# Kernel optimization log

Hardware: AMD Instinct MI355X
Metric: run time of the kernel (lower is better)

Reference implementation:

```python
import jax, jax.numpy as jnp
import numpy as np

D_MODEL = 1024
NHEAD = 16
HEAD_DIM = D_MODEL // NHEAD


def setup_inputs() -> dict:
    key = jax.random.key(0)
    ks = jax.random.split(key, 11)
    B, T = 2, 2048
    s = 1.0 / np.sqrt(D_MODEL)
    return {
        "query": jax.random.normal(ks[0], (B, T, D_MODEL), jnp.float32),
        "key": jax.random.normal(ks[1], (B, T, D_MODEL), jnp.float32),
        "value": jax.random.normal(ks[2], (B, T, D_MODEL), jnp.float32),
        "Wq": jax.random.normal(ks[3], (D_MODEL, D_MODEL), jnp.float32) * s,
        "bq": jnp.zeros((D_MODEL,), jnp.float32),
        "Wk": jax.random.normal(ks[4], (D_MODEL, D_MODEL), jnp.float32) * s,
        "bk": jnp.zeros((D_MODEL,), jnp.float32),
        "Wv": jax.random.normal(ks[5], (D_MODEL, D_MODEL), jnp.float32) * s,
        "bv": jnp.zeros((D_MODEL,), jnp.float32),
        "Wo": jax.random.normal(ks[6], (D_MODEL, D_MODEL), jnp.float32) * s,
        "bo": jnp.zeros((D_MODEL,), jnp.float32),
    }


def reference(query, key, value, Wq, bq, Wk, bk, Wv, bv, Wo, bo):
    B, T, _ = query.shape
    scale = HEAD_DIM ** -0.5
    # Linear projections (torch Linear: x @ W.T + b)
    Q = query @ Wq.T + bq
    K = key @ Wk.T + bk
    V = value @ Wv.T + bv
    # [B, H, T, hd]
    Q = Q.reshape(B, T, NHEAD, HEAD_DIM).transpose(0, 2, 1, 3)
    K = K.reshape(B, T, NHEAD, HEAD_DIM).transpose(0, 2, 1, 3)
    V = V.reshape(B, T, NHEAD, HEAD_DIM).transpose(0, 2, 1, 3)
    # Attention scores [B, H, T, T]
    scores = jnp.einsum("bhqd,bhkd->bhqk", Q, K) * scale
    probs = jax.nn.softmax(scores, axis=-1)
    # dropout is identity in eval mode
    out = jnp.einsum("bhqk,bhkd->bhqd", probs, V)
    out = out.transpose(0, 2, 1, 3).reshape(B, T, D_MODEL)
    return out @ Wo.T + bo
```

## Files before the change

kernel.cpp:

```cpp
#include <hip/hip_runtime.h>
#include <stdint.h>

#define LOG2E_OVER_SQRTHD 0.18033688011112042f
#define SM_BIAS 12.0f

typedef unsigned short u16;
typedef _Float16 f16;
typedef __attribute__((ext_vector_type(4))) float f32x4;
typedef __attribute__((ext_vector_type(8))) _Float16 f16x8;

static __device__ __forceinline__ u16 f2h_bits(float f) {
  union { f16 h; u16 u; } v; v.h = (f16)f; return v.u;
}

static __device__ __forceinline__ void g2l16(const void* g, void* l) {
  __builtin_amdgcn_global_load_lds((const __attribute__((address_space(1))) void*)g,
                                   (__attribute__((address_space(3))) void*)l,
                                   16, 0, 0);
}

__global__ __launch_bounds__(256) void pack_x3(const float* __restrict__ q,
    const float* __restrict__ k, const float* __restrict__ v, u16* __restrict__ dst) {
  int z = blockIdx.y;
  const float* src = (z == 0) ? q : (z == 1) ? k : v;
  u16* d = dst + (size_t)z * 4096 * 1024;
  int idx = blockIdx.x * 256 + threadIdx.x;
  float4 x = ((const float4*)src)[idx];
  ushort4 o;
  o.x = f2h_bits(x.x); o.y = f2h_bits(x.y); o.z = f2h_bits(x.z); o.w = f2h_bits(x.w);
  *(ushort4*)(d + (size_t)idx * 4) = o;
}

__global__ __launch_bounds__(256) void pack_w4(const float* __restrict__ wq,
    const float* __restrict__ wk, const float* __restrict__ wv,
    const float* __restrict__ wo, u16* __restrict__ dst) {
  int z = blockIdx.y;
  const float* src = (z == 0) ? wq : (z == 1) ? wk : (z == 2) ? wv : wo;
  u16* d = dst + (size_t)z * 1024 * 1024;
  int idx = blockIdx.x * 256 + threadIdx.x;
  float4 x = ((const float4*)src)[idx];
  ushort4 o;
  o.x = f2h_bits(x.x); o.y = f2h_bits(x.y); o.z = f2h_bits(x.z); o.w = f2h_bits(x.w);
  *(ushort4*)(d + (size_t)idx * 4) = o;
}

template <bool OUT_F16>
static __device__ __forceinline__ void gemm_body(
    const u16* __restrict__ A, const u16* __restrict__ W,
    const float* __restrict__ bias, void* __restrict__ C, float oscale) {
  __shared__ u16 As[128 * 32];
  __shared__ u16 Bs[128 * 32];
  const int tid = threadIdx.x;
  const int lane = tid & 63;
  const int wave = tid >> 6;
  const int wm = wave >> 1, wn = wave & 1;
  const int quad = lane >> 4, l15 = lane & 15;
  const int bm = blockIdx.x * 128, bn = blockIdx.y * 128;

  f32x4 acc[4][4] = {};

  const int r0 = tid >> 2;
  const int c0 = (tid & 3) * 8;
  const u16* Ab = A + (size_t)bm * 1024;
  const u16* Wb = W + (size_t)bn * 1024;

  for (int kt = 0; kt < 32; ++kt) {
    const int kc = kt * 32;
    g2l16(Ab + (size_t)r0 * 1024 + kc + c0, As + tid * 8);
    g2l16(Ab + (size_t)(r0 + 64) * 1024 + kc + c0, As + (256 + tid) * 8);
    g2l16(Wb + (size_t)r0 * 1024 + kc + c0, Bs + tid * 8);
    g2l16(Wb + (size_t)(r0 + 64) * 1024 + kc + c0, Bs + (256 + tid) * 8);
    __syncthreads();
    f16x8 af[4], bw[4];
#pragma unroll
    for (int mt = 0; mt < 4; ++mt)
      af[mt] = *(const f16x8*)(As + (wm * 64 + mt * 16 + l15) * 32 + quad * 8);
#pragma unroll
    for (int nt = 0; nt < 4; ++nt)
      bw[nt] = *(const f16x8*)(Bs + (wn * 64 + nt * 16 + l15) * 32 + quad * 8);
#pragma unroll
    for (int mt = 0; mt < 4; ++mt)
#pragma unroll
      for (int nt = 0; nt < 4; ++nt)
        acc[mt][nt] = __builtin_amdgcn_mfma_f32_16x16x32_f16(af[mt], bw[nt], acc[mt][nt], 0, 0, 0);
    __syncthreads();
  }

#pragma unroll
  for (int mt = 0; mt < 4; ++mt) {
    const int row = bm + wm * 64 + mt * 16 + quad * 4;
#pragma unroll
    for (int nt = 0; nt < 4; ++nt) {
      const int col = bn + wn * 64 + nt * 16 + l15;
      const float bv = bias[col];
#pragma unroll
      for (int i = 0; i < 4; ++i) {
        float v = (acc[mt][nt][i] + bv) * oscale;
        if (OUT_F16)
          ((u16*)C)[(size_t)(row + i) * 1024 + col] = f2h_bits(v);
        else
          ((float*)C)[(size_t)(row + i) * 1024 + col] = v;
      }
    }
  }
}

__global__ __launch_bounds__(256) void gemm_qkv(const u16* __restrict__ Xf16,
    const u16* __restrict__ Wf16, const float* __restrict__ bq,
    const float* __restrict__ bk, const float* __restrict__ bv,
    u16* __restrict__ QKV, float qscale) {
  int z = blockIdx.z;
  const float* bias = (z == 0) ? bq : (z == 1) ? bk : bv;
  gemm_body<true>(Xf16 + (size_t)z * 4096 * 1024,
                  Wf16 + (size_t)z * 1024 * 1024,
                  bias,
                  QKV + (size_t)z * 4096 * 1024,
                  (z == 0) ? qscale : 1.0f);
}

__global__ __launch_bounds__(256) void gemm_out(const u16* __restrict__ O,
    const u16* __restrict__ Wo, const float* __restrict__ bo,
    float* __restrict__ out) {
  gemm_body<false>(O, Wo, bo, out, 1.0f);
}

__global__ __launch_bounds__(256) void transpose_v(const u16* __restrict__ V,
                                                   u16* __restrict__ Vt) {
  __shared__ u16 Ts[64 * 72];
  const int tid = threadIdx.x;
  const int bi = blockIdx.x;
  const int bj = blockIdx.y;
#pragma unroll
  for (int it = 0; it < 2; ++it) {
    int qq = it * 256 + tid;
    int r = qq >> 3, c = (qq & 7) * 8;
    *(uint4*)(Ts + r * 72 + c) = *(const uint4*)(V + (size_t)(bi * 64 + r) * 1024 + bj * 64 + c);
  }
  __syncthreads();
#pragma unroll
  for (int it = 0; it < 2; ++it) {
    int qq = it * 256 + tid;
    int oc = qq >> 3, k = qq & 7;
    union { uint4 u; u16 s[8]; } w;
#pragma unroll
    for (int j = 0; j < 8; ++j) w.s[j] = Ts[(8 * k + j) * 72 + oc];
    *(uint4*)(Vt + (size_t)(bj * 64 + oc) * 4096 + bi * 64 + 8 * k) = w.u;
  }
}

__global__ __launch_bounds__(256) void attn_kernel(const u16* __restrict__ QKV,
                                                   const u16* __restrict__ Vt,
                                                   u16* __restrict__ O) {
  constexpr int LS = 72;
  constexpr int LSP = 68;
  __shared__ u16 Qs[64 * LS];
  __shared__ u16 Ks[64 * LS];
  __shared__ u16 Vts[64 * LS];
  __shared__ u16 Ps[4][16 * LSP];

  const u16* Qb = QKV;
  const u16* Kb = QKV + (size_t)4096 * 1024;

  const int tid = threadIdx.x, lane = tid & 63, wave = tid >> 6;
  const int quad = lane >> 4, l15 = lane & 15;
  const int qt = blockIdx.x, h = blockIdx.y, b = blockIdx.z;
  const size_t qrow0 = (size_t)b * 2048 + qt * 64;
  const size_t kv0 = (size_t)b * 2048;
  const int hc = h * 64;

  const int sr = tid >> 3;
  const int sc = (tid & 7) * 8;

#pragma unroll
  for (int it = 0; it < 2; ++it) {
    int r = it * 32 + sr;
    *(uint4*)(Qs + r * LS + sc) = *(const uint4*)(Qb + (qrow0 + r) * 1024 + hc + sc);
  }
  __syncthreads();
  const f16x8 aq0 = *(const f16x8*)(Qs + (wave * 16 + l15) * LS + quad * 8);
  const f16x8 aq1 = *(const f16x8*)(Qs + (wave * 16 + l15) * LS + 32 + quad * 8);

  f32x4 o_acc[4] = {};
  float l_part[4] = {0.f, 0.f, 0.f, 0.f};
  u16* Pw = Ps[wave];

  for (int kt = 0; kt < 32; ++kt) {
    const size_t kr0 = kv0 + (size_t)kt * 64;
    __syncthreads();
#pragma unroll
    for (int it = 0; it < 2; ++it) {
      int r = it * 32 + sr;
      *(uint4*)(Ks + r * LS + sc) = *(const uint4*)(Kb + (kr0 + r) * 1024 + hc + sc);
      *(uint4*)(Vts + r * LS + sc) = *(const uint4*)(Vt + (size_t)(hc + r) * 4096 + kr0 + sc);
    }
    __syncthreads();

    f32x4 s[4];
#pragma unroll
    for (int nt = 0; nt < 4; ++nt)
      s[nt] = f32x4{-SM_BIAS, -SM_BIAS, -SM_BIAS, -SM_BIAS};
#pragma unroll
    for (int nt = 0; nt < 4; ++nt) {
      f16x8 bk0 = *(const f16x8*)(Ks + (nt * 16 + l15) * LS + quad * 8);
      f16x8 bk1 = *(const f16x8*)(Ks + (nt * 16 + l15) * LS + 32 + quad * 8);
      s[nt] = __builtin_amdgcn_mfma_f32_16x16x32_f16(aq0, bk0, s[nt], 0, 0, 0);
      s[nt] = __builtin_amdgcn_mfma_f32_16x16x32_f16(aq1, bk1, s[nt], 0, 0, 0);
    }

#pragma unroll
    for (int nt = 0; nt < 4; ++nt)
#pragma unroll
      for (int i = 0; i < 4; ++i) {
        float p = exp2f(s[nt][i]);
        l_part[i] += p;
        Pw[(quad * 4 + i) * LSP + nt * 16 + l15] = f2h_bits(p);
      }
    asm volatile("s_waitcnt lgkmcnt(0)" ::: "memory");

    union { f16x8 v; struct { uint2 lo, hi; } h; } ap0, ap1;
    ap0.h.lo = *(const uint2*)(Pw + l15 * LSP + quad * 8);
    ap0.h.hi = *(const uint2*)(Pw + l15 * LSP + quad * 8 + 4);
    ap1.h.lo = *(const uint2*)(Pw + l15 * LSP + 32 + quad * 8);
    ap1.h.hi = *(const uint2*)(Pw + l15 * LSP + 32 + quad * 8 + 4);
#pragma unroll
    for (int ct = 0; ct < 4; ++ct) {
      f16x8 bv0 = *(const f16x8*)(Vts + (ct * 16 + l15) * LS + quad * 8);
      f16x8 bv1 = *(const f16x8*)(Vts + (ct * 16 + l15) * LS + 32 + quad * 8);
      o_acc[ct] = __builtin_amdgcn_mfma_f32_16x16x32_f16(ap0.v, bv0, o_acc[ct], 0, 0, 0);
      o_acc[ct] = __builtin_amdgcn_mfma_f32_16x16x32_f16(ap1.v, bv1, o_acc[ct], 0, 0, 0);
    }
  }

#pragma unroll
  for (int i = 0; i < 4; ++i)
#pragma unroll
    for (int d = 1; d < 16; d <<= 1) l_part[i] += __shfl_xor(l_part[i], d);

#pragma unroll
  for (int i = 0; i < 4; ++i) {
    const float inv = 1.0f / l_part[i];
    const size_t row = qrow0 + wave * 16 + quad * 4 + i;
#pragma unroll
    for (int ct = 0; ct < 4; ++ct) {
      float ov = o_acc[ct][i] * inv;
      int col = hc + ct * 16 + l15;
      O[row * 1024 + col] = f2h_bits(ov);
    }
  }
}

extern "C" void kernel_launch(void* const* d_in, const int* in_sizes, int n_in,
                              void* d_out, int out_size, void* d_ws, size_t ws_size,
                              hipStream_t stream) {
  const float* query = (const float*)d_in[0];
  const float* key   = (const float*)d_in[1];
  const float* value = (const float*)d_in[2];
  const float* Wq = (const float*)d_in[3];
  const float* bq = (const float*)d_in[4];
  const float* Wk = (const float*)d_in[5];
  const float* bk = (const float*)d_in[6];
  const float* Wv = (const float*)d_in[7];
  const float* bv = (const float*)d_in[8];
  const float* Wo = (const float*)d_in[9];
  const float* bo = (const float*)d_in[10];
  float* out = (float*)d_out;

  u16* Xf16 = (u16*)d_ws;
  u16* Wf16 = Xf16 + (size_t)3 * 4096 * 1024;
  u16* QKV  = Wf16 + (size_t)4 * 1024 * 1024;
  u16* Vt   = Xf16;
  u16* O    = Xf16 + (size_t)1024 * 4096;

  pack_x3<<<dim3(4096, 3, 1), 256, 0, stream>>>(query, key, value, Xf16);
  pack_w4<<<dim3(1024, 4, 1), 256, 0, stream>>>(Wq, Wk, Wv, Wo, Wf16);
  gemm_qkv<<<dim3(32, 8, 3), 256, 0, stream>>>(Xf16, Wf16, bq, bk, bv, QKV,
                                               LOG2E_OVER_SQRTHD);
  transpose_v<<<dim3(64, 16, 1), 256, 0, stream>>>(QKV + (size_t)2 * 4096 * 1024, Vt);
  attn_kernel<<<dim3(32, 16, 2), 256, 0, stream>>>(QKV, Vt, O);
  gemm_out<<<dim3(32, 8, 1), 256, 0, stream>>>(
      O, Wf16 + (size_t)3 * 1024 * 1024, bo, out);
}
```

Measured before the change: 267.7 us.

## Fuse packing kernels, compute V transposed in GEMM, swizzle attention LDS loads

Merges the two fp32-to-fp16 pack kernels into one launch. The V projection is computed as Wv·Xᵀ, so the GEMM writes V already transposed with a per-row bias, and the separate transpose kernel goes away. The attention kernel now stages Q, K and Vt into unpadded LDS with async global_load_lds and an XOR swizzle, and uses the native exp2 intrinsic. This removes two launches and a full V read/write pass and shortens LDS staging, in exchange for a strided row-bias epilogue and extra swizzle index arithmetic.

```diff
diff --git a/kernel.cpp b/kernel.cpp
--- a/kernel.cpp
+++ b/kernel.cpp
@@ -19,35 +19,38 @@
                                    16, 0, 0);
 }
 
-__global__ __launch_bounds__(256) void pack_x3(const float* __restrict__ q,
-    const float* __restrict__ k, const float* __restrict__ v, u16* __restrict__ dst) {
-  int z = blockIdx.y;
-  const float* src = (z == 0) ? q : (z == 1) ? k : v;
-  u16* d = dst + (size_t)z * 4096 * 1024;
-  int idx = blockIdx.x * 256 + threadIdx.x;
+__global__ __launch_bounds__(256) void pack_all(
+    const float* __restrict__ q, const float* __restrict__ k, const float* __restrict__ v,
+    const float* __restrict__ wq, const float* __restrict__ wk,
+    const float* __restrict__ wv, const float* __restrict__ wo,
+    u16* __restrict__ X, u16* __restrict__ W) {
+  int flat = blockIdx.x * 256 + threadIdx.x;
+  const float* src;
+  u16* dst;
+  int idx;
+  if (flat < 3 * 1048576) {
+    int z = flat >> 20;
+    idx = flat & 1048575;
+    src = (z == 0) ? q : (z == 1) ? k : v;
+    dst = X + (size_t)z * 4194304;
+  } else {
+    int f2 = flat - 3 * 1048576;
+    int z = f2 >> 18;
+    idx = f2 & 262143;
+    src = (z == 0) ? wq : (z == 1) ? wk : (z == 2) ? wv : wo;
+    dst = W + (size_t)z * 1048576;
+  }
   float4 x = ((const float4*)src)[idx];
   ushort4 o;
   o.x = f2h_bits(x.x); o.y = f2h_bits(x.y); o.z = f2h_bits(x.z); o.w = f2h_bits(x.w);
-  *(ushort4*)(d + (size_t)idx * 4) = o;
-}
-
-__global__ __launch_bounds__(256) void pack_w4(const float* __restrict__ wq,
-    const float* __restrict__ wk, const float* __restrict__ wv,
-    const float* __restrict__ wo, u16* __restrict__ dst) {
-  int z = blockIdx.y;
-  const float* src = (z == 0) ? wq : (z == 1) ? wk : (z == 2) ? wv : wo;
-  u16* d = dst + (size_t)z * 1024 * 1024;
-  int idx = blockIdx.x * 256 + threadIdx.x;
-  float4 x = ((const float4*)src)[idx];
-  ushort4 o;
-  o.x = f2h_bits(x.x); o.y = f2h_bits(x.y); o.z = f2h_bits(x.z); o.w = f2h_bits(x.w);
-  *(ushort4*)(d + (size_t)idx * 4) = o;
+  *(ushort4*)(dst + (size_t)idx * 4) = o;
 }
 
 template <bool OUT_F16>
 static __device__ __forceinline__ void gemm_body(
     const u16* __restrict__ A, const u16* __restrict__ W,
-    const float* __restrict__ bias, void* __restrict__ C, float oscale) {
+    const float* __restrict__ bias, void* __restrict__ C,
+    int ldc, bool row_bias, float oscale, int bm, int bn) {
   __shared__ u16 As[128 * 32];
   __shared__ u16 Bs[128 * 32];
   const int tid = threadIdx.x;
@@ -55,7 +58,6 @@
   const int wave = tid >> 6;
   const int wm = wave >> 1, wn = wave & 1;
   const int quad = lane >> 4, l15 = lane & 15;
-  const int bm = blockIdx.x * 128, bn = blockIdx.y * 128;
 
   f32x4 acc[4][4] = {};
 
@@ -92,74 +94,57 @@
 #pragma unroll
     for (int nt = 0; nt < 4; ++nt) {
       const int col = bn + wn * 64 + nt * 16 + l15;
-      const float bv = bias[col];
+      const float bcol = row_bias ? 0.0f : bias[col];
 #pragma unroll
       for (int i = 0; i < 4; ++i) {
-        float v = (acc[mt][nt][i] + bv) * oscale;
+        const float bb = row_bias ? bias[row + i] : bcol;
+        float val = (acc[mt][nt][i] + bb) * oscale;
         if (OUT_F16)
-          ((u16*)C)[(size_t)(row + i) * 1024 + col] = f2h_bits(v);
+          ((u16*)C)[(size_t)(row + i) * ldc + col] = f2h_bits(val);
         else
-          ((float*)C)[(size_t)(row + i) * 1024 + col] = v;
+          ((float*)C)[(size_t)(row + i) * ldc + col] = val;
       }
     }
   }
 }
 
-__global__ __launch_bounds__(256) void gemm_qkv(const u16* __restrict__ Xf16,
-    const u16* __restrict__ Wf16, const float* __restrict__ bq,
+__global__ __launch_bounds__(256) void gemm_qkv(const u16* __restrict__ X,
+    const u16* __restrict__ Wf, const float* __restrict__ bq,
     const float* __restrict__ bk, const float* __restrict__ bv,
-    u16* __restrict__ QKV, float qscale) {
-  int z = blockIdx.z;
-  const float* bias = (z == 0) ? bq : (z == 1) ? bk : bv;
-  gemm_body<true>(Xf16 + (size_t)z * 4096 * 1024,
-                  Wf16 + (size_t)z * 1024 * 1024,
-                  bias,
-                  QKV + (size_t)z * 4096 * 1024,
-                  (z == 0) ? qscale : 1.0f);
+    u16* __restrict__ QK, u16* __restrict__ Vt, float qscale) {
+  const int z = blockIdx.z;
+  if (z == 0) {
+    gemm_body<true>(X, Wf, bq, QK, 1024, false, qscale,
+                    blockIdx.x * 128, blockIdx.y * 128);
+  } else if (z == 1) {
+    gemm_body<true>(X + (size_t)4194304, Wf + (size_t)1048576, bk,
+                    QK + (size_t)4194304, 1024, false, 1.0f,
+                    blockIdx.x * 128, blockIdx.y * 128);
+  } else {
+    gemm_body<true>(Wf + (size_t)2 * 1048576, X + (size_t)2 * 4194304, bv,
+                    Vt, 4096, true, 1.0f,
+                    blockIdx.y * 128, blockIdx.x * 128);
+  }
 }
 
 __global__ __launch_bounds__(256) void gemm_out(const u16* __restrict__ O,
     const u16* __restrict__ Wo, const float* __restrict__ bo,
     float* __restrict__ out) {
-  gemm_body<false>(O, Wo, bo, out, 1.0f);
-}
-
-__global__ __launch_bounds__(256) void transpose_v(const u16* __restrict__ V,
-                                                   u16* __restrict__ Vt) {
-  __shared__ u16 Ts[64 * 72];
-  const int tid = threadIdx.x;
-  const int bi = blockIdx.x;
-  const int bj = blockIdx.y;
-#pragma unroll
-  for (int it = 0; it < 2; ++it) {
-    int qq = it * 256 + tid;
-    int r = qq >> 3, c = (qq & 7) * 8;
-    *(uint4*)(Ts + r * 72 + c) = *(const uint4*)(V + (size_t)(bi * 64 + r) * 1024 + bj * 64 + c);
-  }
-  __syncthreads();
-#pragma unroll
-  for (int it = 0; it < 2; ++it) {
-    int qq = it * 256 + tid;
-    int oc = qq >> 3, k = qq & 7;
-    union { uint4 u; u16 s[8]; } w;
-#pragma unroll
-    for (int j = 0; j < 8; ++j) w.s[j] = Ts[(8 * k + j) * 72 + oc];
-    *(uint4*)(Vt + (size_t)(bj * 64 + oc) * 4096 + bi * 64 + 8 * k) = w.u;
-  }
-}
-
-__global__ __launch_bounds__(256) void attn_kernel(const u16* __restrict__ QKV,
+  gemm_body<false>(O, Wo, bo, out, 1024, false, 1.0f,
+                   blockIdx.x * 128, blockIdx.y * 128);
+}
+
+__global__ __launch_bounds__(256) void attn_kernel(const u16* __restrict__ QK,
                                                    const u16* __restrict__ Vt,
                                                    u16* __restrict__ O) {
-  constexpr int LS = 72;
   constexpr int LSP = 68;
-  __shared__ u16 Qs[64 * LS];
-  __shared__ u16 Ks[64 * LS];
-  __shared__ u16 Vts[64 * LS];
+  __shared__ u16 Qs[64 * 64];
+  __shared__ u16 Ks[64 * 64];
+  __shared__ u16 Vts[64 * 64];
   __shared__ u16 Ps[4][16 * LSP];
 
-  const u16* Qb = QKV;
-  const u16* Kb = QKV + (size_t)4096 * 1024;
+  const u16* Qb = QK;
+  const u16* Kb = QK + (size_t)4096 * 1024;
 
   const int tid = threadIdx.x, lane = tid & 63, wave = tid >> 6;
   const int quad = lane >> 4, l15 = lane & 15;
@@ -168,17 +153,17 @@
   const size_t kv0 = (size_t)b * 2048;
   const int hc = h * 64;
 
-  const int sr = tid >> 3;
-  const int sc = (tid & 7) * 8;
-
-#pragma unroll
-  for (int it = 0; it < 2; ++it) {
-    int r = it * 32 + sr;
-    *(uint4*)(Qs + r * LS + sc) = *(const uint4*)(Qb + (qrow0 + r) * 1024 + hc + sc);
-  }
+  const int r0 = tid >> 3;
+  const int p0 = tid & 7;
+  const int s0 = (p0 ^ (r0 & 7)) * 8;
+
+  g2l16(Qb + (qrow0 + r0) * 1024 + hc + s0, Qs + tid * 8);
+  g2l16(Qb + (qrow0 + 32 + r0) * 1024 + hc + s0, Qs + (256 + tid) * 8);
   __syncthreads();
-  const f16x8 aq0 = *(const f16x8*)(Qs + (wave * 16 + l15) * LS + quad * 8);
-  const f16x8 aq1 = *(const f16x8*)(Qs + (wave * 16 + l15) * LS + 32 + quad * 8);
+
+  const int Rq = wave * 16 + l15;
+  const f16x8 aq0 = *(const f16x8*)(Qs + Rq * 64 + ((quad ^ (Rq & 7)) * 8));
+  const f16x8 aq1 = *(const f16x8*)(Qs + Rq * 64 + (((quad + 4) ^ (Rq & 7)) * 8));
 
   f32x4 o_acc[4] = {};
   float l_part[4] = {0.f, 0.f, 0.f, 0.f};
@@ -187,12 +172,10 @@
   for (int kt = 0; kt < 32; ++kt) {
     const size_t kr0 = kv0 + (size_t)kt * 64;
     __syncthreads();
-#pragma unroll
-    for (int it = 0; it < 2; ++it) {
-      int r = it * 32 + sr;
-      *(uint4*)(Ks + r * LS + sc) = *(const uint4*)(Kb + (kr0 + r) * 1024 + hc + sc);
-      *(uint4*)(Vts + r * LS + sc) = *(const uint4*)(Vt + (size_t)(hc + r) * 4096 + kr0 + sc);
-    }
+    g2l16(Kb + (kr0 + r0) * 1024 + hc + s0, Ks + tid * 8);
+    g2l16(Kb + (kr0 + 32 + r0) * 1024 + hc + s0, Ks + (256 + tid) * 8);
+    g2l16(Vt + (size_t)(hc + r0) * 4096 + kr0 + s0, Vts + tid * 8);
+    g2l16(Vt + (size_t)(hc + 32 + r0) * 4096 + kr0 + s0, Vts + (256 + tid) * 8);
     __syncthreads();
 
     f32x4 s[4];
@@ -201,8 +184,9 @@
       s[nt] = f32x4{-SM_BIAS, -SM_BIAS, -SM_BIAS, -SM_BIAS};
 #pragma unroll
     for (int nt = 0; nt < 4; ++nt) {
-      f16x8 bk0 = *(const f16x8*)(Ks + (nt * 16 + l15) * LS + quad * 8);
-      f16x8 bk1 = *(const f16x8*)(Ks + (nt * 16 + l15) * LS + 32 + quad * 8);
+      const int Rk = nt * 16 + l15;
+      f16x8 bk0 = *(const f16x8*)(Ks + Rk * 64 + ((quad ^ (Rk & 7)) * 8));
+      f16x8 bk1 = *(const f16x8*)(Ks + Rk * 64 + (((quad + 4) ^ (Rk & 7)) * 8));
       s[nt] = __builtin_amdgcn_mfma_f32_16x16x32_f16(aq0, bk0, s[nt], 0, 0, 0);
       s[nt] = __builtin_amdgcn_mfma_f32_16x16x32_f16(aq1, bk1, s[nt], 0, 0, 0);
     }
@@ -211,7 +195,7 @@
     for (int nt = 0; nt < 4; ++nt)
 #pragma unroll
       for (int i = 0; i < 4; ++i) {
-        float p = exp2f(s[nt][i]);
+        float p = __builtin_amdgcn_exp2f(s[nt][i]);
         l_part[i] += p;
         Pw[(quad * 4 + i) * LSP + nt * 16 + l15] = f2h_bits(p);
       }
@@ -224,8 +208,9 @@
     ap1.h.hi = *(const uint2*)(Pw + l15 * LSP + 32 + quad * 8 + 4);
 #pragma unroll
     for (int ct = 0; ct < 4; ++ct) {
-      f16x8 bv0 = *(const f16x8*)(Vts + (ct * 16 + l15) * LS + quad * 8);
-      f16x8 bv1 = *(const f16x8*)(Vts + (ct * 16 + l15) * LS + 32 + quad * 8);
+      const int Rv = ct * 16 + l15;
+      f16x8 bv0 = *(const f16x8*)(Vts + Rv * 64 + ((quad ^ (Rv & 7)) * 8));
+      f16x8 bv1 = *(const f16x8*)(Vts + Rv * 64 + (((quad + 4) ^ (Rv & 7)) * 8));
       o_acc[ct] = __builtin_amdgcn_mfma_f32_16x16x32_f16(ap0.v, bv0, o_acc[ct], 0, 0, 0);
       o_acc[ct] = __builtin_amdgcn_mfma_f32_16x16x32_f16(ap1.v, bv1, o_acc[ct], 0, 0, 0);
     }
@@ -265,18 +250,15 @@
   const float* bo = (const float*)d_in[10];
   float* out = (float*)d_out;
 
-  u16* Xf16 = (u16*)d_ws;
-  u16* Wf16 = Xf16 + (size_t)3 * 4096 * 1024;
-  u16* QKV  = Wf16 + (size_t)4 * 1024 * 1024;
-  u16* Vt   = Xf16;
-  u16* O    = Xf16 + (size_t)1024 * 4096;
-
-  pack_x3<<<dim3(4096, 3, 1), 256, 0, stream>>>(query, key, value, Xf16);
-  pack_w4<<<dim3(1024, 4, 1), 256, 0, stream>>>(Wq, Wk, Wv, Wo, Wf16);
-  gemm_qkv<<<dim3(32, 8, 3), 256, 0, stream>>>(Xf16, Wf16, bq, bk, bv, QKV,
+  u16* X  = (u16*)d_ws;
+  u16* W  = X + (size_t)3 * 4194304;
+  u16* QK = W + (size_t)4 * 1048576;
+  u16* Vt = QK + (size_t)2 * 4194304;
+  u16* O  = X;
+
+  pack_all<<<dim3(16384, 1, 1), 256, 0, stream>>>(query, key, value, Wq, Wk, Wv, Wo, X, W);
+  gemm_qkv<<<dim3(32, 8, 3), 256, 0, stream>>>(X, W, bq, bk, bv, QK, Vt,
                                                LOG2E_OVER_SQRTHD);
-  transpose_v<<<dim3(64, 16, 1), 256, 0, stream>>>(QKV + (size_t)2 * 4096 * 1024, Vt);
-  attn_kernel<<<dim3(32, 16, 2), 256, 0, stream>>>(QKV, Vt, O);
-  gemm_out<<<dim3(32, 8, 1), 256, 0, stream>>>(
-      O, Wf16 + (size_t)3 * 1024 * 1024, bo, out);
-}
+  attn_kernel<<<dim3(32, 16, 2), 256, 0, stream>>>(QK, Vt, O);
+  gemm_out<<<dim3(32, 8, 1), 256, 0, stream>>>(O, W + (size_t)3 * 1048576, bo, out);
+}
```

After: 253.3 us. -5.4%, faster.
